# Kernel optimization log

Hardware: AMD Instinct MI355X
Metric: run time of the kernel (lower is better)

Reference implementation:

```python
import jax, jax.numpy as jnp
import numpy as np

D_MODEL = 1024
N_HEADS = 16
D_K = D_MODEL // N_HEADS
LOCAL_WINDOW = 128
GLOBAL_TOKENS = 16


def sparse_mask(seq_len):
    i = jnp.arange(seq_len)[:, None]
    j = jnp.arange(seq_len)[None, :]
    local = jnp.abs(i - j) <= LOCAL_WINDOW
    glob = (i < GLOBAL_TOKENS) | (j < GLOBAL_TOKENS)
    causal = j <= i
    return ((local | glob) & causal)[None, None]  # [1,1,S,S]


def setup_inputs() -> dict:
    key = jax.random.key(0)
    ks = jax.random.split(key, 11)
    B, S = 2, 2048
    std = 1.0 / np.sqrt(D_MODEL)
    inp = {
        'query': jax.random.normal(ks[0], (B, S, D_MODEL), jnp.float32),
        'key': jax.random.normal(ks[1], (B, S, D_MODEL), jnp.float32),
        'value': jax.random.normal(ks[2], (B, S, D_MODEL), jnp.float32),
        'w_q': jax.random.normal(ks[3], (D_MODEL, D_MODEL), jnp.float32) * std,
        'b_q': jnp.zeros((D_MODEL,), jnp.float32),
        'w_k': jax.random.normal(ks[4], (D_MODEL, D_MODEL), jnp.float32) * std,
        'b_k': jnp.zeros((D_MODEL,), jnp.float32),
        'w_v': jax.random.normal(ks[5], (D_MODEL, D_MODEL), jnp.float32) * std,
        'b_v': jnp.zeros((D_MODEL,), jnp.float32),
        'w_o': jax.random.normal(ks[6], (D_MODEL, D_MODEL), jnp.float32) * std,
        'b_o': jnp.zeros((D_MODEL,), jnp.float32),
    }
    return inp


def reference(query, key, value, w_q, b_q, w_k, b_k, w_v, b_v, w_o, b_o):
    B, S, _ = query.shape
    # project and split heads -> [B,H,S,d_k]
    def proj(x, w, b):
        y = x @ w.T + b
        return y.reshape(B, S, N_HEADS, D_K).transpose(0, 2, 1, 3)
    q = proj(query, w_q, b_q)
    k = proj(key, w_k, b_k)
    v = proj(value, w_v, b_v)
    scores = jnp.einsum('bhqd,bhkd->bhqk', q, k) / np.sqrt(D_K).astype(np.float32)
    mask = sparse_mask(S)
    scores = jnp.where(mask, scores, -jnp.inf)
    attn = jax.nn.softmax(scores, axis=-1)
    out = jnp.einsum('bhqk,bhkd->bhqd', attn, v)
    out = out.transpose(0, 2, 1, 3).reshape(B, S, D_MODEL)
    return out @ w_o.T + b_o
```

## Files before the change

kernel.cpp:

```cpp
#include <hip/hip_runtime.h>

typedef unsigned short u16;
typedef u16 u16x8 __attribute__((ext_vector_type(8)));
typedef __bf16 bf16x8 __attribute__((ext_vector_type(8)));
typedef float f32x4 __attribute__((ext_vector_type(4)));

#define MFMA16 __builtin_amdgcn_mfma_f32_16x16x32_bf16

__device__ __forceinline__ u16 f2bf(float f) {
  unsigned u = __builtin_bit_cast(unsigned, f);
  u += 0x7FFFu + ((u >> 16) & 1u);
  return (u16)(u >> 16);
}

__device__ __forceinline__ int swz(int row, int bcol) {
  return row * 128 + (bcol ^ ((row & 7) << 4));
}

__device__ __forceinline__ void gl16(const u16* g, u16* l) {
  __builtin_amdgcn_global_load_lds(
      (const __attribute__((address_space(1))) unsigned int*)g,
      (__attribute__((address_space(3))) unsigned int*)l, 16, 0, 0);
}

__device__ __forceinline__ void BARR() {
  asm volatile("" ::: "memory");
  __builtin_amdgcn_s_barrier();
  asm volatile("" ::: "memory");
}
#define VMCNT(n) asm volatile("s_waitcnt vmcnt(" #n ")" ::: "memory")

__global__ __launch_bounds__(256)
void cast_all(const float* __restrict__ q, const float* __restrict__ k,
              const float* __restrict__ v, const float* __restrict__ wq,
              const float* __restrict__ wk, const float* __restrict__ wv,
              const float* __restrict__ wo, u16* __restrict__ ws) {
  const long i = ((long)blockIdx.x * 256 + threadIdx.x) * 8;
  const float* s;
  u16* d;
  if (i < 12582912) {
    const int seg = (int)(i >> 22);
    const float* xs = (seg == 0) ? q : (seg == 1) ? k : v;
    s = xs + (i & 4194303);
    d = ws + 4194304 + i;
  } else {
    const long j = i - 12582912;
    const int seg = (int)(j >> 20);
    const float* wsrc = (seg == 0) ? wq : (seg == 1) ? wk : (seg == 2) ? wv : wo;
    s = wsrc + (j & 1048575);
    d = ws + j;
  }
  float4 v0 = *(const float4*)s;
  float4 v1 = *(const float4*)(s + 4);
  u16x8 p = {f2bf(v0.x), f2bf(v0.y), f2bf(v0.z), f2bf(v0.w),
             f2bf(v1.x), f2bf(v1.y), f2bf(v1.z), f2bf(v1.w)};
  *(u16x8*)d = p;
}

#define OSTGA(tt, c, j)                                                     \
  gl16(Ain + (m0 + (c)*64 + (w << 4) + (j)*8 + (lane >> 3)) * 1024 +        \
           (tt)*64 + (((lane & 7) ^ (lane >> 3)) << 3),                     \
       (u16*)(sb + (((tt)&1) << 15) + (c)*8192 + (w << 11) + ((j) << 10)))
#define OSTGB(tt, c, j)                                                     \
  gl16(W + (n0 + (c)*64 + (w << 4) + (j)*8 + (lane >> 3)) * 1024 +          \
           (tt)*64 + (((lane & 7) ^ (lane >> 3)) << 3),                     \
       (u16*)(sb + (((tt)&1) << 15) + 16384 + (c)*8192 + (w << 11) +        \
              ((j) << 10)))
#define OLDA()                                                              \
  _Pragma("unroll") for (int m = 0; m < 4; ++m) {                           \
    char* p = sb + bo + rowAb + m * 16 * 128;                               \
    af[0][m] = __builtin_bit_cast(bf16x8, *(const u16x8*)(p + colr0));      \
    af[1][m] = __builtin_bit_cast(bf16x8, *(const u16x8*)(p + colr1));      \
  }
#define OLDB(n)                                                             \
  {                                                                         \
    char* p = sb + bo + rowBb + (n)*16 * 128;                               \
    bf[0][n] = __builtin_bit_cast(bf16x8, *(const u16x8*)(p + colr0));      \
    bf[1][n] = __builtin_bit_cast(bf16x8, *(const u16x8*)(p + colr1));      \
  }
#define OFMA(nh)                                                            \
  __builtin_amdgcn_s_setprio(1);                                            \
  _Pragma("unroll") for (int m = 0; m < 4; ++m)                             \
  _Pragma("unroll") for (int n = 0; n < 2; ++n) {                           \
    acc[m][(nh)*2 + n] =                                                    \
        MFMA16(af[0][m], bf[0][(nh)*2 + n], acc[m][(nh)*2 + n], 0, 0, 0);   \
    acc[m][(nh)*2 + n] =                                                    \
        MFMA16(af[1][m], bf[1][(nh)*2 + n], acc[m][(nh)*2 + n], 0, 0, 0);   \
  }                                                                         \
  __builtin_amdgcn_s_setprio(0);

__device__ __forceinline__ void core128(const u16* __restrict__ Ain,
                                        const u16* __restrict__ W, int m0,
                                        int n0, char* sb,
                                        f32x4 (&acc)[4][4]) {
  const int tid = threadIdx.x, lane = tid & 63, w = tid >> 6;
  const int wm = w >> 1, wn = w & 1;
  const int r = lane & 15, g = lane >> 4;
  bf16x8 af[2][4], bf[2][4];

  const int colr0 = (g * 16) ^ ((r & 7) << 4);
  const int colr1 = (64 + g * 16) ^ ((r & 7) << 4);
  const int rowAb = (wm * 64 + r) * 128;
  const int rowBb = 16384 + (wn * 64 + r) * 128;

#pragma unroll
  for (int c = 0; c < 2; ++c) { OSTGA(0, c, 0); OSTGA(0, c, 1); }
#pragma unroll
  for (int c = 0; c < 2; ++c) { OSTGB(0, c, 0); OSTGB(0, c, 1); }
#pragma unroll
  for (int c = 0; c < 2; ++c) { OSTGA(1, c, 0); OSTGA(1, c, 1); }
  VMCNT(4);
  __builtin_amdgcn_s_barrier();
  asm volatile("" ::: "memory");

  for (int t = 0; t < 16; ++t) {
    const int bo = (t & 1) << 15;
    if (t < 15) { OSTGB(t + 1, 0, 0); OSTGB(t + 1, 0, 1); OSTGB(t + 1, 1, 0); OSTGB(t + 1, 1, 1); }
    OLDA();
    OLDB(0); OLDB(1);
    OFMA(0);
    BARR();
    if (t < 14) { OSTGA(t + 2, 0, 0); OSTGA(t + 2, 0, 1); OSTGA(t + 2, 1, 0); OSTGA(t + 2, 1, 1); }
    OLDB(2); OLDB(3);
    OFMA(1);
    if (t < 14) { VMCNT(4); } else if (t == 14) { VMCNT(0); }
    BARR();
  }
}

__global__ __launch_bounds__(256)
void qkv_gemm128(const u16* __restrict__ ws_in, const float* __restrict__ c0,
                 const float* __restrict__ c1, const float* __restrict__ c2,
                 u16* __restrict__ o0, u16* __restrict__ o1,
                 u16* __restrict__ o2) {
  const int bid = blockIdx.x;
  const int s = (bid & 7) * 96 + (bid >> 3);
  const int z = s >> 8;
  const int rem = s & 255;
  const int m0 = (rem >> 3) << 7, n0 = (rem & 7) << 7;

  const u16* __restrict__ Ain = ws_in + 4194304 + z * 4194304;
  const u16* __restrict__ W = ws_in + z * 1048576;
  const float* Bi = (z == 0) ? c0 : (z == 1) ? c1 : c2;
  u16* O = (z == 0) ? o0 : (z == 1) ? o1 : o2;

  const int tid = threadIdx.x, lane = tid & 63, w = tid >> 6;
  const int wm = w >> 1, wn = w & 1;
  const int r = lane & 15, g = lane >> 4;

  __shared__ u16 SH[32768];
  f32x4 acc[4][4] = {};
  core128(Ain, W, m0, n0, (char*)SH, acc);

#pragma unroll
  for (int n = 0; n < 4; ++n) {
    const int gn = n0 + wn * 64 + n * 16 + r;
    const int hh = gn >> 6, d = gn & 63;
    const float bv = Bi[gn];
#pragma unroll
    for (int m = 0; m < 4; ++m) {
#pragma unroll
      for (int q = 0; q < 4; ++q) {
        int gm = m0 + wm * 64 + m * 16 + g * 4 + q;
        int bb = gm >> 11, sIdx = gm & 2047;
        O[((bb * 16 + hh) * 2048 + sIdx) * 64 + d] = f2bf(acc[m][n][q] + bv);
      }
    }
  }
}

__global__ __launch_bounds__(256)
void out_gemm_p(const u16* __restrict__ Ain2, const u16* __restrict__ W2,
                const float* __restrict__ Bi, float* __restrict__ C) {
  const int bid = blockIdx.x;
  const int s = (bid & 7) * 32 + (bid >> 3);
  const int m0 = (s >> 3) << 7, n0 = (s & 7) << 7;

  const int tid = threadIdx.x, lane = tid & 63, w = tid >> 6;
  const int wm = w >> 1, wn = w & 1;
  const int r = lane & 15, g = lane >> 4;

  __shared__ u16 SH[32768];
  f32x4 acc[4][4] = {};
  core128(Ain2, W2, m0, n0, (char*)SH, acc);

#pragma unroll
  for (int m = 0; m < 4; ++m) {
#pragma unroll
    for (int n = 0; n < 4; ++n) {
      int gn = n0 + wn * 64 + n * 16 + r;
      float bv = Bi[gn];
#pragma unroll
      for (int q = 0; q < 4; ++q) {
        int gm = m0 + wm * 64 + m * 16 + g * 4 + q;
        C[gm * 1024 + gn] = acc[m][n][q] + bv;
      }
    }
  }
}

__global__ __launch_bounds__(256)
void attn_kernel(const u16* __restrict__ Q, const u16* __restrict__ K,
                 const u16* __restrict__ V, u16* __restrict__ O) {
  const int qt = blockIdx.x, h = blockIdx.y, b = blockIdx.z;
  const int tid = threadIdx.x, lane = tid & 63, w = tid >> 6;
  const int r = lane & 15, g = lane >> 4;
  const int q0 = qt * 64;
  const int base = (b * 16 + h) * 131072;
  const u16* Qb = Q + base;
  const u16* Kb = K + base;
  const u16* Vb = V + base;

  __shared__ u16 Ks[64 * 64];
  __shared__ u16 Vt[64 * 64];
  __shared__ u16 Pl[4608];

  bf16x8 qf[2];
  {
    const u16* qp = Qb + (q0 + w * 16 + r) * 64 + g * 8;
    qf[0] = __builtin_bit_cast(bf16x8, *(const u16x8*)qp);
    qf[1] = __builtin_bit_cast(bf16x8, *(const u16x8*)(qp + 32));
  }

  f32x4 acc[4] = {};
  float m_run[4] = {-1e30f, -1e30f, -1e30f, -1e30f};
  float l_run[4] = {};

  const int nt = (qt <= 3) ? (qt + 1) : 4;
  const int srow = tid >> 3, sc = (tid & 7) * 8;

  for (int tix = 0; tix < nt; ++tix) {
    const int t = (tix == 0) ? 0 : ((qt <= 3) ? tix : (qt - 3 + tix));
    const int j0 = t * 64;
    __syncthreads();
#pragma unroll
    for (int i = 0; i < 2; ++i) {
      int row = i * 32 + srow;
      u16x8 kv = *(const u16x8*)(Kb + (j0 + row) * 64 + sc);
      *(u16x8*)((char*)Ks + swz(row, sc * 2)) = kv;
      u16x8 vv = *(const u16x8*)(Vb + (j0 + row) * 64 + sc);
#pragma unroll
      for (int qq = 0; qq < 8; ++qq) {
        int d = sc + qq;
        *(u16*)((char*)Vt + d * 128 + ((2 * row) ^ ((d & 7) << 4))) = vv[qq];
      }
    }
    __syncthreads();

    f32x4 S[4] = {};
#pragma unroll
    for (int kk = 0; kk < 2; ++kk)
#pragma unroll
      for (int n = 0; n < 4; ++n) {
        bf16x8 kf = __builtin_bit_cast(
            bf16x8,
            *(const u16x8*)((char*)Ks + swz(n * 16 + r, kk * 64 + g * 16)));
        S[n] = MFMA16(qf[kk], kf, S[n], 0, 0, 0);
      }

    float mloc[4] = {-1e30f, -1e30f, -1e30f, -1e30f};
#pragma unroll
    for (int n = 0; n < 4; ++n) {
      int j = j0 + n * 16 + r;
#pragma unroll
      for (int q = 0; q < 4; ++q) {
        int i = q0 + w * 16 + g * 4 + q;
        bool ok = (j <= i) && (((i - j) <= 128) || (j < 16));
        float s = ok ? S[n][q] * 0.125f : -1e30f;
        S[n][q] = s;
        mloc[q] = fmaxf(mloc[q], s);
      }
    }
#pragma unroll
    for (int q = 0; q < 4; ++q)
#pragma unroll
      for (int off = 1; off < 16; off <<= 1)
        mloc[q] = fmaxf(mloc[q], __shfl_xor(mloc[q], off));

    float alpha[4], rsum[4] = {};
#pragma unroll
    for (int q = 0; q < 4; ++q) {
      float mn = fmaxf(m_run[q], mloc[q]);
      alpha[q] = __expf(m_run[q] - mn);
      m_run[q] = mn;
    }
#pragma unroll
    for (int n = 0; n < 4; ++n)
#pragma unroll
      for (int q = 0; q < 4; ++q) {
        float p = __expf(S[n][q] - m_run[q]);
        S[n][q] = p;
        rsum[q] += p;
      }
#pragma unroll
    for (int q = 0; q < 4; ++q) {
#pragma unroll
      for (int off = 1; off < 16; off <<= 1)
        rsum[q] += __shfl_xor(rsum[q], off);
      l_run[q] = l_run[q] * alpha[q] + rsum[q];
    }
#pragma unroll
    for (int n = 0; n < 4; ++n) {
      acc[n][0] *= alpha[0];
      acc[n][1] *= alpha[1];
      acc[n][2] *= alpha[2];
      acc[n][3] *= alpha[3];
    }

#pragma unroll
    for (int n = 0; n < 4; ++n)
#pragma unroll
      for (int q = 0; q < 4; ++q)
        *((u16*)((char*)Pl + w * 2304 + (g * 4 + q) * 144) + (n * 16 + r)) =
            f2bf(S[n][q]);

#pragma unroll
    for (int kk = 0; kk < 2; ++kk) {
      bf16x8 pf = __builtin_bit_cast(
          bf16x8,
          *(const u16x8*)((char*)Pl + w * 2304 + r * 144 + kk * 64 + g * 16));
#pragma unroll
      for (int n = 0; n < 4; ++n) {
        bf16x8 vf = __builtin_bit_cast(
            bf16x8,
            *(const u16x8*)((char*)Vt + swz(n * 16 + r, kk * 64 + g * 16)));
        acc[n] = MFMA16(pf, vf, acc[n], 0, 0, 0);
      }
    }
  }

#pragma unroll
  for (int n = 0; n < 4; ++n)
#pragma unroll
    for (int q = 0; q < 4; ++q) {
      int s = q0 + w * 16 + g * 4 + q;
      int d = n * 16 + r;
      O[(b * 2048 + s) * 1024 + h * 64 + d] = f2bf(acc[n][q] / l_run[q]);
    }
}

extern "C" void kernel_launch(void* const* d_in, const int* in_sizes, int n_in,
                              void* d_out, int out_size, void* d_ws,
                              size_t ws_size, hipStream_t stream) {
  const float* b_q = (const float*)d_in[4];
  const float* b_k = (const float*)d_in[6];
  const float* b_v = (const float*)d_in[8];
  const float* b_o = (const float*)d_in[10];

  u16* ws = (u16*)d_ws;
  u16* Qw = ws + 16777216;
  u16* Kw = ws + 20971520;
  u16* Vw = ws + 25165824;
  u16* Aw = ws + 4194304;

  cast_all<<<dim3(8192), dim3(256), 0, stream>>>(
      (const float*)d_in[0], (const float*)d_in[1], (const float*)d_in[2],
      (const float*)d_in[3], (const float*)d_in[5], (const float*)d_in[7],
      (const float*)d_in[9], ws);
  qkv_gemm128<<<dim3(768), dim3(256), 0, stream>>>(ws, b_q, b_k, b_v, Qw, Kw,
                                                   Vw);
  attn_kernel<<<dim3(32, 16, 2), dim3(256), 0, stream>>>(Qw, Kw, Vw, Aw);
  out_gemm_p<<<dim3(256), dim3(256), 0, stream>>>(Aw, ws + 3145728, b_o,
                                                  (float*)d_out);
}
```

Baseline: 93.16 us.

## Replace QKV GEMM with 256x256-tile, 8-wave kernel using quadrant pipelining

Replaces the 128x128-tile QKV projection GEMM (768 blocks of 4 waves) with a 256x256-tile kernel (192 blocks of 8 waves) that uses 128KB of LDS with double buffering. The main loop is split into four quadrant phases, and global-to-LDS loads for the next tiles are interleaved between them with finer vmcnt waits and barriers. Larger tiles raise arithmetic intensity and cut redundant global reads of A and W. In exchange, only 192 blocks are launched on a 256-CU device, leaving some CUs idle, and each block uses more registers and LDS.

Result: no change. 94.60 us (+1.5%).

```diff
diff --git a/kernel.cpp b/kernel.cpp
--- a/kernel.cpp
+++ b/kernel.cpp
@@ -57,6 +57,139 @@
   *(u16x8*)d = p;
 }
 
+__global__ __launch_bounds__(512)
+void qkv8p(const u16* __restrict__ ws_in, const float* __restrict__ c0,
+           const float* __restrict__ c1, const float* __restrict__ c2,
+           u16* __restrict__ o0, u16* __restrict__ o1,
+           u16* __restrict__ o2) {
+  const int bid = blockIdx.x;
+  const int s = (bid & 7) * 24 + (bid >> 3);
+  const int z = s >> 6;
+  const int rem = s & 63;
+  const int m0 = (rem >> 2) << 8;
+  const int n0 = (rem & 3) << 8;
+
+  const u16* __restrict__ A = ws_in + 4194304 + z * 4194304;
+  const u16* __restrict__ W = ws_in + z * 1048576;
+  const float* Bi = (z == 0) ? c0 : (z == 1) ? c1 : c2;
+  u16* O = (z == 0) ? o0 : (z == 1) ? o1 : o2;
+
+  const int tid = threadIdx.x, lane = tid & 63, w = tid >> 6;
+  const int wm = w >> 2, wn = w & 3;
+  const int r = lane & 15, g = lane >> 4;
+
+  __shared__ u16 SH[65536];
+  char* sb = (char*)SH;
+
+  f32x4 acc[8][4] = {};
+  bf16x8 afr[2][4], bfr[2][2];
+
+  const u16* Asrc = A + (m0 + (w << 3) + (lane >> 3)) * 1024 +
+                    (((lane & 7) ^ (lane >> 3)) << 3);
+  const u16* Bsrc = W + (n0 + (w << 3) + (lane >> 3)) * 1024 +
+                    (((lane & 7) ^ (lane >> 3)) << 3);
+  u16* Adst = (u16*)SH + (w << 9);
+  u16* Bdst = (u16*)SH + 32768 + (w << 9);
+
+#define STA8(tt, h)                                                         \
+  {                                                                         \
+    gl16(Asrc + (h)*131072 + (tt)*64, Adst + (((tt)&1) << 14) + ((h) << 13)); \
+    gl16(Asrc + (h)*131072 + 65536 + (tt)*64,                               \
+         Adst + (((tt)&1) << 14) + ((h) << 13) + 4096);                     \
+  }
+#define STB8(tt, h)                                                         \
+  {                                                                         \
+    gl16(Bsrc + (h)*131072 + (tt)*64, Bdst + (((tt)&1) << 14) + ((h) << 13)); \
+    gl16(Bsrc + (h)*131072 + 65536 + (tt)*64,                               \
+         Bdst + (((tt)&1) << 14) + ((h) << 13) + 4096);                     \
+  }
+
+  const int colr0 = (g * 16) ^ ((r & 7) << 4);
+  const int colr1 = (64 + g * 16) ^ ((r & 7) << 4);
+  const int rowA = (wm * 16 + r) * 128;
+  const int rowB = (wn * 16 + r) * 128;
+
+#define LDSA(qm)                                                            \
+  _Pragma("unroll") for (int i = 0; i < 4; ++i) {                           \
+    char* p = sb + bo + (qm)*16384 + rowA + i * 4096;                       \
+    afr[0][i] = __builtin_bit_cast(bf16x8, *(const u16x8*)(p + colr0));     \
+    afr[1][i] = __builtin_bit_cast(bf16x8, *(const u16x8*)(p + colr1));     \
+  }
+#define LDSB(qn)                                                            \
+  _Pragma("unroll") for (int jj = 0; jj < 2; ++jj) {                        \
+    char* p = sb + bo + 65536 + (qn)*16384 + rowB + jj * 8192;              \
+    bfr[0][jj] = __builtin_bit_cast(bf16x8, *(const u16x8*)(p + colr0));    \
+    bfr[1][jj] = __builtin_bit_cast(bf16x8, *(const u16x8*)(p + colr1));    \
+  }
+#define FMAQ(qm, qn)                                                        \
+  __builtin_amdgcn_s_setprio(1);                                            \
+  _Pragma("unroll") for (int i = 0; i < 4; ++i)                             \
+  _Pragma("unroll") for (int jj = 0; jj < 2; ++jj) {                        \
+    acc[(qm)*4 + i][(qn)*2 + jj] = MFMA16(afr[0][i], bfr[0][jj],            \
+                                          acc[(qm)*4 + i][(qn)*2 + jj], 0,  \
+                                          0, 0);                            \
+    acc[(qm)*4 + i][(qn)*2 + jj] = MFMA16(afr[1][i], bfr[1][jj],            \
+                                          acc[(qm)*4 + i][(qn)*2 + jj], 0,  \
+                                          0, 0);                            \
+  }                                                                         \
+  __builtin_amdgcn_s_setprio(0);
+
+  STA8(0, 0);
+  STB8(0, 0);
+  STA8(0, 1);
+  STB8(0, 1);
+  STA8(1, 0);
+  STB8(1, 0);
+  VMCNT(8);
+  __builtin_amdgcn_s_barrier();
+  asm volatile("" ::: "memory");
+
+  for (int t = 0; t < 16; ++t) {
+    const int bo = (t & 1) << 15;
+    if (t < 15) STA8(t + 1, 1);
+    LDSA(0);
+    LDSB(0);
+    FMAQ(0, 0);
+    if (t < 15) { VMCNT(6); } else { VMCNT(0); }
+    BARR();
+    if (t < 15) STB8(t + 1, 1);
+    LDSB(1);
+    FMAQ(0, 1);
+    BARR();
+    if (t < 14) STA8(t + 2, 0);
+    LDSA(1);
+    LDSB(0);
+    FMAQ(1, 0);
+    BARR();
+    if (t < 14) STB8(t + 2, 0);
+    LDSB(1);
+    FMAQ(1, 1);
+    if (t < 14) { VMCNT(6); } else if (t == 14) { VMCNT(4); }
+    BARR();
+  }
+
+#pragma unroll
+  for (int j = 0; j < 4; ++j) {
+    const int gn = n0 + j * 64 + wn * 16 + r;
+    const int hh = gn >> 6, d = gn & 63;
+    const float bv = Bi[gn];
+#pragma unroll
+    for (int f = 0; f < 8; ++f) {
+#pragma unroll
+      for (int q = 0; q < 4; ++q) {
+        int gm = m0 + f * 32 + wm * 16 + g * 4 + q;
+        int bb = gm >> 11, sIdx = gm & 2047;
+        O[((bb * 16 + hh) * 2048 + sIdx) * 64 + d] = f2bf(acc[f][j][q] + bv);
+      }
+    }
+  }
+#undef STA8
+#undef STB8
+#undef LDSA
+#undef LDSB
+#undef FMAQ
+}
+
 #define OSTGA(tt, c, j)                                                     \
   gl16(Ain + (m0 + (c)*64 + (w << 4) + (j)*8 + (lane >> 3)) * 1024 +        \
            (tt)*64 + (((lane & 7) ^ (lane >> 3)) << 3),                     \
@@ -129,47 +262,6 @@
 }
 
 __global__ __launch_bounds__(256)
-void qkv_gemm128(const u16* __restrict__ ws_in, const float* __restrict__ c0,
-                 const float* __restrict__ c1, const float* __restrict__ c2,
-                 u16* __restrict__ o0, u16* __restrict__ o1,
-                 u16* __restrict__ o2) {
-  const int bid = blockIdx.x;
-  const int s = (bid & 7) * 96 + (bid >> 3);
-  const int z = s >> 8;
-  const int rem = s & 255;
-  const int m0 = (rem >> 3) << 7, n0 = (rem & 7) << 7;
-
-  const u16* __restrict__ Ain = ws_in + 4194304 + z * 4194304;
-  const u16* __restrict__ W = ws_in + z * 1048576;
-  const float* Bi = (z == 0) ? c0 : (z == 1) ? c1 : c2;
-  u16* O = (z == 0) ? o0 : (z == 1) ? o1 : o2;
-
-  const int tid = threadIdx.x, lane = tid & 63, w = tid >> 6;
-  const int wm = w >> 1, wn = w & 1;
-  const int r = lane & 15, g = lane >> 4;
-
-  __shared__ u16 SH[32768];
-  f32x4 acc[4][4] = {};
-  core128(Ain, W, m0, n0, (char*)SH, acc);
-
-#pragma unroll
-  for (int n = 0; n < 4; ++n) {
-    const int gn = n0 + wn * 64 + n * 16 + r;
-    const int hh = gn >> 6, d = gn & 63;
-    const float bv = Bi[gn];
-#pragma unroll
-    for (int m = 0; m < 4; ++m) {
-#pragma unroll
-      for (int q = 0; q < 4; ++q) {
-        int gm = m0 + wm * 64 + m * 16 + g * 4 + q;
-        int bb = gm >> 11, sIdx = gm & 2047;
-        O[((bb * 16 + hh) * 2048 + sIdx) * 64 + d] = f2bf(acc[m][n][q] + bv);
-      }
-    }
-  }
-}
-
-__global__ __launch_bounds__(256)
 void out_gemm_p(const u16* __restrict__ Ain2, const u16* __restrict__ W2,
                 const float* __restrict__ Bi, float* __restrict__ C) {
   const int bid = blockIdx.x;
@@ -357,8 +449,7 @@
       (const float*)d_in[0], (const float*)d_in[1], (const float*)d_in[2],
       (const float*)d_in[3], (const float*)d_in[5], (const float*)d_in[7],
       (const float*)d_in[9], ws);
-  qkv_gemm128<<<dim3(768), dim3(256), 0, stream>>>(ws, b_q, b_k, b_v, Qw, Kw,
-                                                   Vw);
+  qkv8p<<<dim3(192), dim3(512), 0, stream>>>(ws, b_q, b_k, b_v, Qw, Kw, Vw);
   attn_kernel<<<dim3(32, 16, 2), dim3(256), 0, stream>>>(Qw, Kw, Vw, Aw);
   out_gemm_p<<<dim3(256), dim3(256), 0, stream>>>(Aw, ws + 3145728, b_o,
                                                   (float*)d_out);
```

## Fuse fp32-to-bf16 activation cast into QKV projection GEMM

Applied to the files above, without the earlier changes.

The separate cast of query/key/value to bf16 is removed. The QKV GEMM now loads fp32 activations into registers, converts them to bf16, and writes them to swizzled LDS, with a register double-buffered pipeline alongside direct-to-LDS weight loads. This avoids writing and re-reading 12M bf16 activation elements through global memory. In exchange, fp32 loads double the A-side read bytes per tile and add register pressure and conversion ALU work inside the GEMM loop.

After: 103.9 us. +11.6%, slower.

```diff
diff --git a/kernel.cpp b/kernel.cpp
--- a/kernel.cpp
+++ b/kernel.cpp
@@ -29,32 +29,176 @@
   asm volatile("" ::: "memory");
 }
 #define VMCNT(n) asm volatile("s_waitcnt vmcnt(" #n ")" ::: "memory")
+#define LGKM0 asm volatile("s_waitcnt lgkmcnt(0)" ::: "memory")
+#define FENCE asm volatile("" ::: "memory")
 
 __global__ __launch_bounds__(256)
-void cast_all(const float* __restrict__ q, const float* __restrict__ k,
-              const float* __restrict__ v, const float* __restrict__ wq,
-              const float* __restrict__ wk, const float* __restrict__ wv,
-              const float* __restrict__ wo, u16* __restrict__ ws) {
-  const long i = ((long)blockIdx.x * 256 + threadIdx.x) * 8;
-  const float* s;
-  u16* d;
-  if (i < 12582912) {
-    const int seg = (int)(i >> 22);
-    const float* xs = (seg == 0) ? q : (seg == 1) ? k : v;
-    s = xs + (i & 4194303);
-    d = ws + 4194304 + i;
-  } else {
-    const long j = i - 12582912;
-    const int seg = (int)(j >> 20);
-    const float* wsrc = (seg == 0) ? wq : (seg == 1) ? wk : (seg == 2) ? wv : wo;
-    s = wsrc + (j & 1048575);
-    d = ws + j;
-  }
+void cast_w(const float* __restrict__ wq, const float* __restrict__ wk,
+            const float* __restrict__ wv, const float* __restrict__ wo,
+            u16* __restrict__ ws) {
+  const int i = (blockIdx.x * 256 + threadIdx.x) * 8;
+  const int seg = i >> 20;
+  const float* s =
+      ((seg == 0) ? wq : (seg == 1) ? wk : (seg == 2) ? wv : wo) + (i & 1048575);
   float4 v0 = *(const float4*)s;
   float4 v1 = *(const float4*)(s + 4);
   u16x8 p = {f2bf(v0.x), f2bf(v0.y), f2bf(v0.z), f2bf(v0.w),
              f2bf(v1.x), f2bf(v1.y), f2bf(v1.z), f2bf(v1.w)};
-  *(u16x8*)d = p;
+  *(u16x8*)(ws + i) = p;
+}
+
+__global__ __launch_bounds__(256)
+void qkv_f32a(const float* __restrict__ Xq, const float* __restrict__ Xk,
+              const float* __restrict__ Xv, const u16* __restrict__ Wall,
+              const float* __restrict__ bq, const float* __restrict__ bk,
+              const float* __restrict__ bv, u16* __restrict__ Qw,
+              u16* __restrict__ Kw, u16* __restrict__ Vw) {
+  const int bid = blockIdx.x;
+  const int sw = (bid & 7) * 96 + (bid >> 3);
+  const int z = sw >> 8;
+  const int rem = sw & 255;
+  const int m0 = (rem >> 3) << 7, n0 = (rem & 7) << 7;
+
+  const float* __restrict__ X = (z == 0) ? Xq : (z == 1) ? Xk : Xv;
+  const u16* __restrict__ Wp = Wall + z * 1048576;
+  const float* Bi = (z == 0) ? bq : (z == 1) ? bk : bv;
+  u16* O = (z == 0) ? Qw : (z == 1) ? Kw : Vw;
+
+  const int tid = threadIdx.x, lane = tid & 63, w = tid >> 6;
+  const int wm = w >> 1, wn = w & 1;
+  const int r = lane & 15, g = lane >> 4;
+
+  __shared__ u16 SH[32768];
+  char* sb = (char*)SH;
+
+  f32x4 acc[4][4] = {};
+  bf16x8 af[2][4], bf[2][4];
+  float4 rE[8], rO[8];
+
+  const int colr0 = (g * 16) ^ ((r & 7) << 4);
+  const int colr1 = (64 + g * 16) ^ ((r & 7) << 4);
+  const int rowAb = (wm * 64 + r) * 128;
+  const int rowBb = 16384 + (wn * 64 + r) * 128;
+  const int arow = tid >> 3;
+  const int acolb = (tid & 7) * 16;
+  const int aswz = acolb ^ ((arow & 7) << 4);
+  const float* Xbase = X + (m0 + arow) * 1024 + (tid & 7) * 8;
+
+#define ISSUEA(regs, tt)                                                    \
+  {                                                                         \
+    FENCE;                                                                  \
+    _Pragma("unroll") for (int c = 0; c < 4; ++c) {                         \
+      const float* xp = Xbase + c * 32768 + (tt)*64;                        \
+      regs[2 * c] = *(const float4*)xp;                                     \
+      regs[2 * c + 1] = *(const float4*)(xp + 4);                           \
+    }                                                                       \
+    FENCE;                                                                  \
+  }
+#define WRITEA(regs, bufb)                                                  \
+  _Pragma("unroll") for (int c = 0; c < 4; ++c) {                           \
+    u16x8 pk = {f2bf(regs[2 * c].x),     f2bf(regs[2 * c].y),               \
+                f2bf(regs[2 * c].z),     f2bf(regs[2 * c].w),               \
+                f2bf(regs[2 * c + 1].x), f2bf(regs[2 * c + 1].y),           \
+                f2bf(regs[2 * c + 1].z), f2bf(regs[2 * c + 1].w)};          \
+    *(u16x8*)(sb + (bufb) + (c * 32 + arow) * 128 + aswz) = pk;             \
+  }
+#define QSTGB(tt)                                                           \
+  {                                                                         \
+    FENCE;                                                                  \
+    _Pragma("unroll") for (int c = 0; c < 2; ++c)                           \
+        _Pragma("unroll") for (int jj = 0; jj < 2; ++jj)                    \
+            gl16(Wp + (n0 + c * 64 + (w << 4) + jj * 8 + (lane >> 3)) * 1024 + \
+                     (tt)*64 + (((lane & 7) ^ (lane >> 3)) << 3),           \
+                 (u16*)(sb + (((tt)&1) << 15) + 16384 + c * 8192 +          \
+                        (w << 11) + (jj << 10)));                           \
+    FENCE;                                                                  \
+  }
+#define QLDA(bo)                                                            \
+  _Pragma("unroll") for (int m = 0; m < 4; ++m) {                           \
+    char* p = sb + (bo) + rowAb + m * 16 * 128;                             \
+    af[0][m] = __builtin_bit_cast(bf16x8, *(const u16x8*)(p + colr0));      \
+    af[1][m] = __builtin_bit_cast(bf16x8, *(const u16x8*)(p + colr1));      \
+  }
+#define QLDB(bo, n)                                                         \
+  {                                                                         \
+    char* p = sb + (bo) + rowBb + (n)*16 * 128;                             \
+    bf[0][n] = __builtin_bit_cast(bf16x8, *(const u16x8*)(p + colr0));      \
+    bf[1][n] = __builtin_bit_cast(bf16x8, *(const u16x8*)(p + colr1));      \
+  }
+#define QFMA(nh)                                                            \
+  __builtin_amdgcn_s_setprio(1);                                            \
+  _Pragma("unroll") for (int m = 0; m < 4; ++m)                             \
+  _Pragma("unroll") for (int n = 0; n < 2; ++n) {                           \
+    acc[m][(nh)*2 + n] =                                                    \
+        MFMA16(af[0][m], bf[0][(nh)*2 + n], acc[m][(nh)*2 + n], 0, 0, 0);   \
+    acc[m][(nh)*2 + n] =                                                    \
+        MFMA16(af[1][m], bf[1][(nh)*2 + n], acc[m][(nh)*2 + n], 0, 0, 0);   \
+  }                                                                         \
+  __builtin_amdgcn_s_setprio(0);
+
+  ISSUEA(rE, 0);
+  QSTGB(0);
+  ISSUEA(rO, 1);
+  WRITEA(rE, 0);
+  VMCNT(8);
+  LGKM0;
+  __builtin_amdgcn_s_barrier();
+  FENCE;
+
+#pragma unroll 1
+  for (int u = 0; u < 8; ++u) {
+    const int t0 = 2 * u, t1 = 2 * u + 1;
+    if (t0 < 15) QSTGB(t0 + 1);
+    if (t0 < 14) ISSUEA(rE, t0 + 2);
+    QLDA(0);
+    QLDB(0, 0);
+    QLDB(0, 1);
+    QFMA(0);
+    BARR();
+    if (t0 < 15) WRITEA(rO, 32768);
+    QLDB(0, 2);
+    QLDB(0, 3);
+    QFMA(1);
+    if (t0 < 14) { VMCNT(8); } else { VMCNT(0); }
+    LGKM0;
+    BARR();
+    if (t1 < 15) QSTGB(t1 + 1);
+    if (t1 < 14) ISSUEA(rO, t1 + 2);
+    QLDA(32768);
+    QLDB(32768, 0);
+    QLDB(32768, 1);
+    QFMA(0);
+    BARR();
+    if (t1 < 15) WRITEA(rE, 0);
+    QLDB(32768, 2);
+    QLDB(32768, 3);
+    QFMA(1);
+    if (t1 < 14) { VMCNT(8); } else if (t1 == 14) { VMCNT(0); }
+    if (t1 < 15) LGKM0;
+    BARR();
+  }
+
+#pragma unroll
+  for (int n = 0; n < 4; ++n) {
+    const int gn = n0 + wn * 64 + n * 16 + r;
+    const int hh = gn >> 6, d = gn & 63;
+    const float bv = Bi[gn];
+#pragma unroll
+    for (int m = 0; m < 4; ++m) {
+#pragma unroll
+      for (int q = 0; q < 4; ++q) {
+        int gm = m0 + wm * 64 + m * 16 + g * 4 + q;
+        int bb = gm >> 11, sIdx = gm & 2047;
+        O[((bb * 16 + hh) * 2048 + sIdx) * 64 + d] = f2bf(acc[m][n][q] + bv);
+      }
+    }
+  }
+#undef ISSUEA
+#undef WRITEA
+#undef QSTGB
+#undef QLDA
+#undef QLDB
+#undef QFMA
 }
 
 #define OSTGA(tt, c, j)                                                     \
@@ -129,47 +273,6 @@
 }
 
 __global__ __launch_bounds__(256)
-void qkv_gemm128(const u16* __restrict__ ws_in, const float* __restrict__ c0,
-                 const float* __restrict__ c1, const float* __restrict__ c2,
-                 u16* __restrict__ o0, u16* __restrict__ o1,
-                 u16* __restrict__ o2) {
-  const int bid = blockIdx.x;
-  const int s = (bid & 7) * 96 + (bid >> 3);
-  const int z = s >> 8;
-  const int rem = s & 255;
-  const int m0 = (rem >> 3) << 7, n0 = (rem & 7) << 7;
-
-  const u16* __restrict__ Ain = ws_in + 4194304 + z * 4194304;
-  const u16* __restrict__ W = ws_in + z * 1048576;
-  const float* Bi = (z == 0) ? c0 : (z == 1) ? c1 : c2;
-  u16* O = (z == 0) ? o0 : (z == 1) ? o1 : o2;
-
-  const int tid = threadIdx.x, lane = tid & 63, w = tid >> 6;
-  const int wm = w >> 1, wn = w & 1;
-  const int r = lane & 15, g = lane >> 4;
-
-  __shared__ u16 SH[32768];
-  f32x4 acc[4][4] = {};
-  core128(Ain, W, m0, n0, (char*)SH, acc);
-
-#pragma unroll
-  for (int n = 0; n < 4; ++n) {
-    const int gn = n0 + wn * 64 + n * 16 + r;
-    const int hh = gn >> 6, d = gn & 63;
-    const float bv = Bi[gn];
-#pragma unroll
-    for (int m = 0; m < 4; ++m) {
-#pragma unroll
-      for (int q = 0; q < 4; ++q) {
-        int gm = m0 + wm * 64 + m * 16 + g * 4 + q;
-        int bb = gm >> 11, sIdx = gm & 2047;
-        O[((bb * 16 + hh) * 2048 + sIdx) * 64 + d] = f2bf(acc[m][n][q] + bv);
-      }
-    }
-  }
-}
-
-__global__ __launch_bounds__(256)
 void out_gemm_p(const u16* __restrict__ Ain2, const u16* __restrict__ W2,
                 const float* __restrict__ Bi, float* __restrict__ C) {
   const int bid = blockIdx.x;
@@ -342,23 +445,25 @@
 extern "C" void kernel_launch(void* const* d_in, const int* in_sizes, int n_in,
                               void* d_out, int out_size, void* d_ws,
                               size_t ws_size, hipStream_t stream) {
+  const float* query = (const float*)d_in[0];
+  const float* key = (const float*)d_in[1];
+  const float* value = (const float*)d_in[2];
   const float* b_q = (const float*)d_in[4];
   const float* b_k = (const float*)d_in[6];
   const float* b_v = (const float*)d_in[8];
   const float* b_o = (const float*)d_in[10];
 
   u16* ws = (u16*)d_ws;
-  u16* Qw = ws + 16777216;
-  u16* Kw = ws + 20971520;
-  u16* Vw = ws + 25165824;
-  u16* Aw = ws + 4194304;
-
-  cast_all<<<dim3(8192), dim3(256), 0, stream>>>(
-      (const float*)d_in[0], (const float*)d_in[1], (const float*)d_in[2],
+  u16* Qw = ws + 4194304;
+  u16* Kw = ws + 8388608;
+  u16* Vw = ws + 12582912;
+  u16* Aw = ws + 16777216;
+
+  cast_w<<<dim3(2048), dim3(256), 0, stream>>>(
       (const float*)d_in[3], (const float*)d_in[5], (const float*)d_in[7],
       (const float*)d_in[9], ws);
-  qkv_gemm128<<<dim3(768), dim3(256), 0, stream>>>(ws, b_q, b_k, b_v, Qw, Kw,
-                                                   Vw);
+  qkv_f32a<<<dim3(768), dim3(256), 0, stream>>>(query, key, value, ws, b_q,
+                                                b_k, b_v, Qw, Kw, Vw);
   attn_kernel<<<dim3(32, 16, 2), dim3(256), 0, stream>>>(Qw, Kw, Vw, Aw);
   out_gemm_p<<<dim3(256), dim3(256), 0, stream>>>(Aw, ws + 3145728, b_o,
                                                   (float*)d_out);
```

## Double-buffer K/V tiles in LDS with register prefetch in attention

Applied to the files above, without the earlier changes.

The attention loop now keeps two LDS buffers for K and transposed V. The next tile's global loads are issued into registers before the current tile is computed, which removes one of the two barriers per iteration. The aim is to hide global load latency behind the MFMA and softmax work. In exchange it uses more LDS and registers, which may reduce occupancy.

After: 92.72 us. Within noise of the previous version (-0.5%).

```diff
diff --git a/kernel.cpp b/kernel.cpp
--- a/kernel.cpp
+++ b/kernel.cpp
@@ -29,6 +29,7 @@
   asm volatile("" ::: "memory");
 }
 #define VMCNT(n) asm volatile("s_waitcnt vmcnt(" #n ")" ::: "memory")
+#define LGKM0 asm volatile("s_waitcnt lgkmcnt(0)" ::: "memory")
 
 __global__ __launch_bounds__(256)
 void cast_all(const float* __restrict__ q, const float* __restrict__ k,
@@ -208,11 +209,9 @@
   const int q0 = qt * 64;
   const int base = (b * 16 + h) * 131072;
   const u16* Qb = Q + base;
-  const u16* Kb = K + base;
-  const u16* Vb = V + base;
-
-  __shared__ u16 Ks[64 * 64];
-  __shared__ u16 Vt[64 * 64];
+
+  __shared__ u16 Ks[2][4096];
+  __shared__ u16 Vt[2][4096];
   __shared__ u16 Pl[4608];
 
   bf16x8 qf[2];
@@ -228,103 +227,141 @@
 
   const int nt = (qt <= 3) ? (qt + 1) : 4;
   const int srow = tid >> 3, sc = (tid & 7) * 8;
-
-  for (int tix = 0; tix < nt; ++tix) {
-    const int t = (tix == 0) ? 0 : ((qt <= 3) ? tix : (qt - 3 + tix));
-    const int j0 = t * 64;
-    __syncthreads();
-#pragma unroll
-    for (int i = 0; i < 2; ++i) {
-      int row = i * 32 + srow;
-      u16x8 kv = *(const u16x8*)(Kb + (j0 + row) * 64 + sc);
-      *(u16x8*)((char*)Ks + swz(row, sc * 2)) = kv;
-      u16x8 vv = *(const u16x8*)(Vb + (j0 + row) * 64 + sc);
-#pragma unroll
-      for (int qq = 0; qq < 8; ++qq) {
-        int d = sc + qq;
-        *(u16*)((char*)Vt + d * 128 + ((2 * row) ^ ((d & 7) << 4))) = vv[qq];
-      }
-    }
-    __syncthreads();
-
-    f32x4 S[4] = {};
-#pragma unroll
-    for (int kk = 0; kk < 2; ++kk)
+  const u16* Kg = K + base + srow * 64 + sc;
+  const u16* Vg = V + base + srow * 64 + sc;
+
+  u16x8 krA[2], vrA[2], krB[2], vrB[2];
+  krA[0] = *(const u16x8*)(Kg);
+  krA[1] = *(const u16x8*)(Kg + 2048);
+  vrA[0] = *(const u16x8*)(Vg);
+  vrA[1] = *(const u16x8*)(Vg + 2048);
+
+#pragma unroll
+  for (int tix = 0; tix < 4; ++tix) {
+    if (tix < nt) {
+      const int j0 = ((tix == 0) ? 0 : ((qt <= 3) ? tix : (qt - 3 + tix))) * 64;
+      const int bo = (tix & 1) * 8192;
+      if ((tix & 1) == 0) {
+#pragma unroll
+        for (int i = 0; i < 2; ++i) {
+          int row = i * 32 + srow;
+          *(u16x8*)((char*)Ks + bo + swz(row, sc * 2)) = krA[i];
+#pragma unroll
+          for (int qq = 0; qq < 8; ++qq) {
+            int d = sc + qq;
+            *(u16*)((char*)Vt + bo + d * 128 + ((2 * row) ^ ((d & 7) << 4))) =
+                vrA[i][qq];
+          }
+        }
+      } else {
+#pragma unroll
+        for (int i = 0; i < 2; ++i) {
+          int row = i * 32 + srow;
+          *(u16x8*)((char*)Ks + bo + swz(row, sc * 2)) = krB[i];
+#pragma unroll
+          for (int qq = 0; qq < 8; ++qq) {
+            int d = sc + qq;
+            *(u16*)((char*)Vt + bo + d * 128 + ((2 * row) ^ ((d & 7) << 4))) =
+                vrB[i][qq];
+          }
+        }
+      }
+      if (tix + 1 < nt) {
+        const int jn = (((qt <= 3) ? (tix + 1) : (qt - 2 + tix)) * 64) * 64;
+        if ((tix & 1) == 0) {
+          krB[0] = *(const u16x8*)(Kg + jn);
+          krB[1] = *(const u16x8*)(Kg + jn + 2048);
+          vrB[0] = *(const u16x8*)(Vg + jn);
+          vrB[1] = *(const u16x8*)(Vg + jn + 2048);
+        } else {
+          krA[0] = *(const u16x8*)(Kg + jn);
+          krA[1] = *(const u16x8*)(Kg + jn + 2048);
+          vrA[0] = *(const u16x8*)(Vg + jn);
+          vrA[1] = *(const u16x8*)(Vg + jn + 2048);
+        }
+      }
+      LGKM0;
+      BARR();
+
+      f32x4 S[4] = {};
+#pragma unroll
+      for (int kk = 0; kk < 2; ++kk)
+#pragma unroll
+        for (int n = 0; n < 4; ++n) {
+          bf16x8 kf = __builtin_bit_cast(
+              bf16x8, *(const u16x8*)((char*)Ks + bo +
+                                      swz(n * 16 + r, kk * 64 + g * 16)));
+          S[n] = MFMA16(qf[kk], kf, S[n], 0, 0, 0);
+        }
+
+      float mloc[4] = {-1e30f, -1e30f, -1e30f, -1e30f};
 #pragma unroll
       for (int n = 0; n < 4; ++n) {
-        bf16x8 kf = __builtin_bit_cast(
-            bf16x8,
-            *(const u16x8*)((char*)Ks + swz(n * 16 + r, kk * 64 + g * 16)));
-        S[n] = MFMA16(qf[kk], kf, S[n], 0, 0, 0);
-      }
-
-    float mloc[4] = {-1e30f, -1e30f, -1e30f, -1e30f};
-#pragma unroll
-    for (int n = 0; n < 4; ++n) {
-      int j = j0 + n * 16 + r;
+        int j = j0 + n * 16 + r;
+#pragma unroll
+        for (int q = 0; q < 4; ++q) {
+          int i = q0 + w * 16 + g * 4 + q;
+          bool ok = (j <= i) && (((i - j) <= 128) || (j < 16));
+          float s = ok ? S[n][q] * 0.125f : -1e30f;
+          S[n][q] = s;
+          mloc[q] = fmaxf(mloc[q], s);
+        }
+      }
+#pragma unroll
+      for (int q = 0; q < 4; ++q)
+#pragma unroll
+        for (int off = 1; off < 16; off <<= 1)
+          mloc[q] = fmaxf(mloc[q], __shfl_xor(mloc[q], off));
+
+      float alpha[4], rsum[4] = {};
 #pragma unroll
       for (int q = 0; q < 4; ++q) {
-        int i = q0 + w * 16 + g * 4 + q;
-        bool ok = (j <= i) && (((i - j) <= 128) || (j < 16));
-        float s = ok ? S[n][q] * 0.125f : -1e30f;
-        S[n][q] = s;
-        mloc[q] = fmaxf(mloc[q], s);
-      }
-    }
-#pragma unroll
-    for (int q = 0; q < 4; ++q)
-#pragma unroll
-      for (int off = 1; off < 16; off <<= 1)
-        mloc[q] = fmaxf(mloc[q], __shfl_xor(mloc[q], off));
-
-    float alpha[4], rsum[4] = {};
-#pragma unroll
-    for (int q = 0; q < 4; ++q) {
-      float mn = fmaxf(m_run[q], mloc[q]);
-      alpha[q] = __expf(m_run[q] - mn);
-      m_run[q] = mn;
-    }
-#pragma unroll
-    for (int n = 0; n < 4; ++n)
+        float mn = fmaxf(m_run[q], mloc[q]);
+        alpha[q] = __expf(m_run[q] - mn);
+        m_run[q] = mn;
+      }
+#pragma unroll
+      for (int n = 0; n < 4; ++n)
+#pragma unroll
+        for (int q = 0; q < 4; ++q) {
+          float p = __expf(S[n][q] - m_run[q]);
+          S[n][q] = p;
+          rsum[q] += p;
+        }
 #pragma unroll
       for (int q = 0; q < 4; ++q) {
-        float p = __expf(S[n][q] - m_run[q]);
-        S[n][q] = p;
-        rsum[q] += p;
-      }
-#pragma unroll
-    for (int q = 0; q < 4; ++q) {
-#pragma unroll
-      for (int off = 1; off < 16; off <<= 1)
-        rsum[q] += __shfl_xor(rsum[q], off);
-      l_run[q] = l_run[q] * alpha[q] + rsum[q];
-    }
-#pragma unroll
-    for (int n = 0; n < 4; ++n) {
-      acc[n][0] *= alpha[0];
-      acc[n][1] *= alpha[1];
-      acc[n][2] *= alpha[2];
-      acc[n][3] *= alpha[3];
-    }
-
-#pragma unroll
-    for (int n = 0; n < 4; ++n)
-#pragma unroll
-      for (int q = 0; q < 4; ++q)
-        *((u16*)((char*)Pl + w * 2304 + (g * 4 + q) * 144) + (n * 16 + r)) =
-            f2bf(S[n][q]);
-
-#pragma unroll
-    for (int kk = 0; kk < 2; ++kk) {
-      bf16x8 pf = __builtin_bit_cast(
-          bf16x8,
-          *(const u16x8*)((char*)Pl + w * 2304 + r * 144 + kk * 64 + g * 16));
+#pragma unroll
+        for (int off = 1; off < 16; off <<= 1)
+          rsum[q] += __shfl_xor(rsum[q], off);
+        l_run[q] = l_run[q] * alpha[q] + rsum[q];
+      }
 #pragma unroll
       for (int n = 0; n < 4; ++n) {
-        bf16x8 vf = __builtin_bit_cast(
-            bf16x8,
-            *(const u16x8*)((char*)Vt + swz(n * 16 + r, kk * 64 + g * 16)));
-        acc[n] = MFMA16(pf, vf, acc[n], 0, 0, 0);
+        acc[n][0] *= alpha[0];
+        acc[n][1] *= alpha[1];
+        acc[n][2] *= alpha[2];
+        acc[n][3] *= alpha[3];
+      }
+
+#pragma unroll
+      for (int n = 0; n < 4; ++n)
+#pragma unroll
+        for (int q = 0; q < 4; ++q)
+          *((u16*)((char*)Pl + w * 2304 + (g * 4 + q) * 144) + (n * 16 + r)) =
+              f2bf(S[n][q]);
+
+#pragma unroll
+      for (int kk = 0; kk < 2; ++kk) {
+        bf16x8 pf = __builtin_bit_cast(
+            bf16x8, *(const u16x8*)((char*)Pl + w * 2304 + r * 144 + kk * 64 +
+                                    g * 16));
+#pragma unroll
+        for (int n = 0; n < 4; ++n) {
+          bf16x8 vf = __builtin_bit_cast(
+              bf16x8, *(const u16x8*)((char*)Vt + bo +
+                                      swz(n * 16 + r, kk * 64 + g * 16)));
+          acc[n] = MFMA16(pf, vf, acc[n], 0, 0, 0);
+        }
       }
     }
   }
```
